# Kernel optimization log

Measured on AMD Instinct MI355X. Metric: run time of the kernel, lower is better.

Reference implementation:

```python
import jax, jax.numpy as jnp
import numpy as np
import math

B, N, E, H = 2, 2048, 1024, 16
D = E // H

def setup_inputs() -> dict:
    key = jax.random.key(0)
    ks = jax.random.split(key, 9)
    s = 1.0 / math.sqrt(E)
    return {
        "x": jax.random.normal(ks[0], (B, N, E), dtype=jnp.float32),
        "Wq": jax.random.uniform(ks[1], (E, E), jnp.float32, -s, s),
        "bq": jax.random.uniform(ks[2], (E,), jnp.float32, -s, s),
        "Wk": jax.random.uniform(ks[3], (E, E), jnp.float32, -s, s),
        "bk": jax.random.uniform(ks[4], (E,), jnp.float32, -s, s),
        "Wv": jax.random.uniform(ks[5], (E, E), jnp.float32, -s, s),
        "bv": jax.random.uniform(ks[6], (E,), jnp.float32, -s, s),
        "Wo": jax.random.uniform(ks[7], (E, E), jnp.float32, -s, s),
        "bo": jax.random.uniform(ks[8], (E,), jnp.float32, -s, s),
    }

def _split_heads(t):
    # [b, n, (h d)] -> [b, h, n, d]
    b, n, _ = t.shape
    return t.reshape(b, n, H, D).transpose(0, 2, 1, 3)

def reference(x, Wq, bq, Wk, bk, Wv, bv, Wo, bo):
    q = _split_heads(x @ Wq.T + bq)
    k = _split_heads(x @ Wk.T + bk)
    v = _split_heads(x @ Wv.T + bv)
    energy = jnp.einsum('bhqd,bhkd->bhqk', q, k)
    # Faithful to source: softmax first, THEN divide by sqrt(n_embedding)
    attention = jax.nn.softmax(energy, axis=-1) / jnp.sqrt(jnp.float32(E))
    out = jnp.einsum('bhqk,bhkd->bhqd', attention, v)
    out = out.transpose(0, 2, 1, 3).reshape(x.shape[0], x.shape[1], E)
    return out @ Wo.T + bo
```

## Files before the change

kernel.cpp:

```cpp
#include <hip/hip_runtime.h>


typedef __bf16 bf16x8 __attribute__((ext_vector_type(8)));
typedef float  f32x4  __attribute__((ext_vector_type(4)));
typedef float  f32x16 __attribute__((ext_vector_type(16)));
using u16 = unsigned short;
using u32 = unsigned int;
typedef u16 u16x8 __attribute__((ext_vector_type(8)));
typedef u16 u16x4 __attribute__((ext_vector_type(4)));
typedef u32 u32x4 __attribute__((ext_vector_type(4)));

constexpr int BATCH = 2, SEQ = 2048, EMB = 1024, NH = 16, HD = 64;
constexpr int MTOT = BATCH * SEQ;
constexpr int KTOT = EMB;
constexpr int NTOT = EMB;
constexpr float LOG2E = 1.44269504088896340736f;

constexpr size_t OFF_XBF = 0;
constexpr size_t OFF_WQ  = 8u * 1024 * 1024;
constexpr size_t OFF_WK  = OFF_WQ + 2u * 1024 * 1024;
constexpr size_t OFF_WV  = OFF_WK + 2u * 1024 * 1024;
constexpr size_t OFF_WO  = OFF_WV + 2u * 1024 * 1024;
constexpr size_t OFF_Q   = OFF_WO + 2u * 1024 * 1024;
constexpr size_t OFF_K   = OFF_Q  + 8u * 1024 * 1024;
constexpr size_t OFF_VT  = OFF_K  + 8u * 1024 * 1024;

__device__ __forceinline__ u16 f2bf(float f) {
  u32 u = __builtin_bit_cast(u32, f);
  u = (u + 0x7fffu + ((u >> 16) & 1u)) >> 16;
  return (u16)u;
}

__device__ __forceinline__ bf16x8 ld_bf16x8(const u16* p) {
  return __builtin_bit_cast(bf16x8, *(const u16x8*)p);
}

__device__ __forceinline__ float fexp2(float x) {
#if __has_builtin(__builtin_amdgcn_exp2f)
  return __builtin_amdgcn_exp2f(x);
#else
  return exp2f(x);
#endif
}

__device__ __forceinline__ float fmax3(float a, float b, float c) {
  float d;
  asm("v_max3_f32 %0, %1, %2, %3" : "=v"(d) : "v"(a), "v"(b), "v"(c));
  return d;
}

__device__ __forceinline__ u32 cvtpk(float lo, float hi_) {
  u32 r;
  asm("v_cvt_pk_bf16_f32 %0, %1, %2" : "=v"(r) : "v"(lo), "v"(hi_));
  return r;
}

__device__ __forceinline__ void stage16(const void* g, void* l) {
#if __has_builtin(__builtin_amdgcn_global_load_lds)
  __builtin_amdgcn_global_load_lds(
      (__attribute__((address_space(1))) void*)const_cast<void*>(g),
      (__attribute__((address_space(3))) void*)l, 16, 0, 0);
#else
  int lane = threadIdx.x & 63;
  uint4 v = *(const uint4*)g;
  *(uint4*)((char*)l + lane * 16) = v;
#endif
}

__global__ __launch_bounds__(256) void cvt_all(
    const float* __restrict__ x, const float* __restrict__ wq,
    const float* __restrict__ wk, const float* __restrict__ wv,
    const float* __restrict__ wo, u16* __restrict__ ox, u16* __restrict__ oq,
    u16* __restrict__ okk, u16* __restrict__ ov, u16* __restrict__ oo) {
  int id = blockIdx.x;
  const float* in;
  u16* out;
  int i;
  if (id < 4096) {
    in = x; out = ox; i = id * 256 + threadIdx.x;
  } else {
    int z = (id - 4096) >> 10, r = (id - 4096) & 1023;
    in = (z == 0) ? wq : (z == 1) ? wk : (z == 2) ? wv : wo;
    out = (z == 0) ? oq : (z == 1) ? okk : (z == 2) ? ov : oo;
    i = r * 256 + threadIdx.x;
  }
  float4 f = ((const float4*)in)[i];
  u32 lo = (u32)f2bf(f.x) | ((u32)f2bf(f.y) << 16);
  u32 hi = (u32)f2bf(f.z) | ((u32)f2bf(f.w) << 16);
  ((uint2*)out)[i] = make_uint2(lo, hi);
}

__device__ __forceinline__ void gemm_bt_core(const u16* __restrict__ A,
                                             const u16* __restrict__ Bm,
                                             const float* __restrict__ bias,
                                             void* __restrict__ out, int mode,
                                             float oscale) {
  __shared__ __align__(16) u16 smem[2][2][128 * 32];
  const int tid = threadIdx.x, w = tid >> 6, ln = tid & 63;
  const int wr = w >> 1, wc = w & 1, qq = ln >> 4, t = ln & 15;
  const int m0 = blockIdx.y * 128, n0 = blockIdx.x * 128;

  f32x4 acc[2][4] = {};

#define GSTAGE(bi, kt)                                                         \
  {                                                                            \
    int ck = w * 64 + ln;                                          \
    int r = ck >> 2, c2 = ck & 3;                                              \
    stage16(&A[(size_t)(m0 + r) * KTOT + (kt) + c2 * 8],                       \
            &smem[bi][0][(size_t)(w * 64) * 8]);                               \
    stage16(&Bm[(size_t)(n0 + r) * KTOT + (kt) + c2 * 8],                      \
            &smem[bi][1][(size_t)(w * 64) * 8]);                               \
  }

  GSTAGE(0, 0)
  __syncthreads();

  int bs = 0;
  for (int kt = 0; kt < KTOT; kt += 32, bs ^= 1) {
    if (kt + 32 < KTOT) GSTAGE(bs ^ 1, kt + 32)
    const u16* sA = smem[bs][0];
    const u16* sB = smem[bs][1];

    bf16x8 av[2], bv[4];
#pragma unroll
    for (int f = 0; f < 2; f++)
      av[f] = ld_bf16x8(&sA[(wr * 32 + f * 16 + t) * 32 + qq * 8]);
#pragma unroll
    for (int f = 0; f < 4; f++)
      bv[f] = ld_bf16x8(&sB[(wc * 64 + f * 16 + t) * 32 + qq * 8]);
#pragma unroll
    for (int i = 0; i < 2; i++)
#pragma unroll
      for (int j = 0; j < 4; j++)
        acc[i][j] = __builtin_amdgcn_mfma_f32_16x16x32_bf16(av[i], bv[j], acc[i][j], 0, 0, 0);
    __syncthreads();
  }
#undef GSTAGE

  if (mode == 1) {
    u16* tb = (u16*)smem;
    const int b = m0 >> 11;
    const int t16 = tid & 15;
    const int tokb = (m0 & 2047) + t16 * 8;
#pragma unroll
    for (int ph = 0; ph < 2; ph++) {
      if (ph == 1) __syncthreads();
      if (wc == ph) {
#pragma unroll
        for (int fc = 0; fc < 4; fc++) {
          int nl = fc * 16 + t;
          float bn = bias[n0 + ph * 64 + nl];
#pragma unroll
          for (int fr = 0; fr < 2; fr++)
#pragma unroll
            for (int i = 0; i < 4; i++) {
              int ml = wr * 32 + fr * 16 + qq * 4 + i;
              tb[nl * 128 + (ml ^ ((nl & 7) << 4))] = f2bf(acc[fr][fc][i] + bn);
            }
        }
      }
      __syncthreads();
#pragma unroll
      for (int p = 0; p < 2; p++) {
        int row = p * 32 + (tid >> 4);
        int n = n0 + ph * 64 + row;
        int hh = n >> 6, d = n & 63;
        u16x8 vd = *(const u16x8*)&tb[row * 128 + ((t16 * 8) ^ ((row & 7) << 4))];
        *(u16x8*)&((u16*)out)[(((size_t)(b * NH + hh)) * HD + d) * SEQ + tokb] = vd;
      }
    }
    return;
  }

#pragma unroll
  for (int fc = 0; fc < 4; fc++) {
    int n = n0 + wc * 64 + fc * 16 + t;
    float bn = bias[n];
#pragma unroll
    for (int fr = 0; fr < 2; fr++) {
#pragma unroll
      for (int i = 0; i < 4; i++) {
        int m = m0 + wr * 32 + fr * 16 + qq * 4 + i;
        float v = (acc[fr][fc][i] + bn) * oscale;
        if (mode == 2) {
          ((float*)out)[(size_t)m * NTOT + n] = v;
        } else {
          int b = m >> 11, tok = m & 2047, h = n >> 6, d = n & 63;
          ((u16*)out)[(((size_t)(b * NH + h)) * SEQ + tok) * HD + d] = f2bf(v);
        }
      }
    }
  }
}

__global__ __launch_bounds__(512) void gemm_qkv(
    const u16* __restrict__ A, const u16* __restrict__ WQ, const u16* __restrict__ WK,
    const u16* __restrict__ WV, const float* __restrict__ bq, const float* __restrict__ bk,
    const float* __restrict__ bv, u16* Qo, u16* Ko, u16* Vo) {
  int z = blockIdx.z;
  const u16* Bm = (z == 0) ? WQ : ((z == 1) ? WK : WV);
  const float* bias = (z == 0) ? bq : ((z == 1) ? bk : bv);
  u16* out = (z == 0) ? Qo : ((z == 1) ? Ko : Vo);
  gemm_bt_core(A, Bm, bias, out, (z == 2) ? 1 : 0, (z == 0) ? LOG2E : 1.0f);
}

__global__ __launch_bounds__(512) void gemm_o(const u16* __restrict__ A,
                                              const u16* __restrict__ WO,
                                              const float* __restrict__ bo,
                                              float* __restrict__ out) {
  gemm_bt_core(A, WO, bo, out, 2, 1.0f);
}

__global__ __launch_bounds__(512, 4) void flash_attn(const u16* __restrict__ Q,
                                                     const u16* __restrict__ Kg,
                                                     const u16* __restrict__ VT,
                                                     u16* __restrict__ O) {
  const int e = blockIdx.x;
  const int xcd = e & 7, slot = e >> 3;
  const int bh = xcd * 4 + (slot & 3);
  const int qt = slot >> 2;

  const int tid = threadIdx.x, w = tid >> 6, ln = tid & 63;
  const int c = ln & 31, hi = ln >> 5;
  const int kb = w >> 2;
  const int q0 = qt * 128 + (w & 3) * 32;

  const u16* Qb = Q + (size_t)bh * SEQ * HD;
  const u16* Kb = Kg + (size_t)bh * SEQ * HD;
  const u16* Vb = VT + (size_t)bh * HD * SEQ;

  __shared__ __align__(16) u16 sK[2][64 * 64];
  __shared__ __align__(16) u16 sV[2][64 * 64];
  __shared__ float2 sml[8][64];

  bf16x8 qf[4];
#pragma unroll
  for (int ks = 0; ks < 4; ks++)
    qf[ks] = ld_bf16x8(&Qb[(size_t)(q0 + c) * HD + ks * 16 + hi * 8]);

  const bf16x8 ones = __builtin_bit_cast(
      bf16x8, (u16x8){0x3f80, 0x3f80, 0x3f80, 0x3f80, 0x3f80, 0x3f80, 0x3f80, 0x3f80});

  f32x16 ot[2];
  ot[0] = 0.f; ot[1] = 0.f;
  f32x16 acc_l = 0.f;
  float m = -1e30f;

#define STAGE(buf, kt)                                                         \
  {                                                                            \
    int ck = w * 64 + ln;                                                      \
    int r = ck >> 3, c2 = ck & 7, c2s = c2 ^ (r & 7);                          \
    stage16(&Kb[(size_t)((kt) + r) * HD + c2s * 8],                            \
            &sK[buf][(size_t)(w * 64) * 8]);                                   \
    stage16(&Vb[(size_t)r * SEQ + (kt) + c2s * 8],                             \
            &sV[buf][(size_t)(w * 64) * 8]);                                   \
  }

  STAGE(0, 0)
  __syncthreads();

  int it = 0;
  for (int kt = 0; kt < SEQ; kt += 64, it ^= 1) {
    if (kt + 64 < SEQ) STAGE(it ^ 1, kt + 64)
    const u16* kbuf = sK[it];
    const u16* vbuf = sV[it];

    f32x16 st = 0.f;
    __builtin_amdgcn_s_setprio(1);
#pragma unroll
    for (int ks = 0; ks < 4; ks++) {
      int row = kb * 32 + c;
      int boff = ((2 * ks + hi) ^ (row & 7)) << 4;
      bf16x8 kf = ld_bf16x8((const u16*)((const char*)(kbuf + row * 64) + boff));
      st = __builtin_amdgcn_mfma_f32_32x32x16_bf16(kf, qf[ks], st, 0, 0, 0);
    }
    __builtin_amdgcn_s_setprio(0);

    float a0 = fmax3(st[0], st[1], st[2]);
    float a1 = fmax3(st[3], st[4], st[5]);
    float a2 = fmax3(st[6], st[7], st[8]);
    float a3 = fmax3(st[9], st[10], st[11]);
    float a4 = fmax3(st[12], st[13], st[14]);
    float a5 = fmaxf(st[15], a0);
    float b0 = fmax3(a1, a2, a3);
    float b1 = fmax3(a4, a5, b0);
    float pmax = fmaxf(b1, __shfl_xor(b1, 32));

    if (!__all(pmax <= m + 8.0f)) {
      float mn = fmaxf(m, pmax);
      float sc = fexp2(m - mn);
      acc_l[0] *= sc;
#pragma unroll
      for (int i = 0; i < 16; i++) { ot[0][i] *= sc; ot[1][i] *= sc; }
      m = mn;
    }

#pragma unroll
    for (int i = 0; i < 16; i++) st[i] = fexp2(st[i] - m);

    bf16x8 pb[2];
#pragma unroll
    for (int ks2 = 0; ks2 < 2; ks2++) {
      const int R0 = 8 * ks2;
      const int R1 = 4 * ((2 * ks2 + 1) & 3);
      u32 X0 = cvtpk(st[R0], st[R0 + 1]);
      u32 X1 = cvtpk(st[R0 + 2], st[R0 + 3]);
      u32 Y0 = cvtpk(st[R1], st[R1 + 1]);
      u32 Y1 = cvtpk(st[R1 + 2], st[R1 + 3]);
      asm("v_permlane32_swap_b32 %0, %1" : "+v"(X0), "+v"(Y0));
      asm("v_permlane32_swap_b32 %0, %1" : "+v"(X1), "+v"(Y1));
      u32x4 wd; wd.x = X0; wd.y = X1; wd.z = Y0; wd.w = Y1;
      pb[ks2] = __builtin_bit_cast(bf16x8, wd);
    }

    __builtin_amdgcn_s_setprio(1);
#pragma unroll
    for (int ks2 = 0; ks2 < 2; ks2++) {
#pragma unroll
      for (int db = 0; db < 2; db++) {
        int row = db * 32 + c;
        int boff = ((kb * 4 + ks2 * 2 + hi) ^ (row & 7)) << 4;
        bf16x8 vf = ld_bf16x8((const u16*)((const char*)(vbuf + row * 64) + boff));
        ot[db] = __builtin_amdgcn_mfma_f32_32x32x16_bf16(vf, pb[ks2], ot[db], 0, 0, 0);
      }
      acc_l = __builtin_amdgcn_mfma_f32_32x32x16_bf16(ones, pb[ks2], acc_l, 0, 0, 0);
    }
    __builtin_amdgcn_s_setprio(0);
    __syncthreads();
  }
#undef STAGE

  float myl = acc_l[0];
  const int pair = w & 3;
  float* xA = (float*)sK;
  float* xB = (float*)sV;
  {
    f32x16 give = (w < 4) ? ot[1] : ot[0];
    *(f32x16*)((w < 4 ? xA : xB) + (size_t)(pair * 64 + ln) * 16) = give;
    sml[w][ln] = make_float2(m, myl);
  }
  __syncthreads();

  float2 po = sml[w ^ 4][ln];
  float M2 = fmaxf(m, po.x);
  float s_me = fexp2(m - M2), s_po = fexp2(po.x - M2);
  float lf = myl * s_me + po.y * s_po;
  float inv = 1.0f / (lf * 32.0f);
  f32x16 oth = *(const f32x16*)((w < 4 ? xB : xA) + (size_t)(pair * 64 + ln) * 16);
  f32x16 own = (w < 4) ? ot[0] : ot[1];
  const int db = (w < 4) ? 0 : 1;

  const int b = bh >> 4, h = bh & 15;
  u16* obase = O + ((size_t)(b * SEQ + q0 + c)) * EMB + h * HD;
#pragma unroll
  for (int g = 0; g < 4; g++) {
    u16x4 pkt;
#pragma unroll
    for (int i = 0; i < 4; i++)
      pkt[i] = f2bf((own[g * 4 + i] * s_me + oth[g * 4 + i] * s_po) * inv);
    *(u16x4*)(obase + db * 32 + g * 8 + hi * 4) = pkt;
  }
}

extern "C" void kernel_launch(void* const* d_in, const int* in_sizes, int n_in,
                              void* d_out, int out_size, void* d_ws, size_t ws_size,
                              hipStream_t stream) {
  const float* x  = (const float*)d_in[0];
  const float* Wq = (const float*)d_in[1];
  const float* bq = (const float*)d_in[2];
  const float* Wk = (const float*)d_in[3];
  const float* bk = (const float*)d_in[4];
  const float* Wv = (const float*)d_in[5];
  const float* bv = (const float*)d_in[6];
  const float* Wo = (const float*)d_in[7];
  const float* bo = (const float*)d_in[8];

  char* ws = (char*)d_ws;
  u16* xbf = (u16*)(ws + OFF_XBF);
  u16* wqb = (u16*)(ws + OFF_WQ);
  u16* wkb = (u16*)(ws + OFF_WK);
  u16* wvb = (u16*)(ws + OFF_WV);
  u16* wob = (u16*)(ws + OFF_WO);
  u16* Qw  = (u16*)(ws + OFF_Q);
  u16* Kw  = (u16*)(ws + OFF_K);
  u16* Vw  = (u16*)(ws + OFF_VT);

  cvt_all<<<dim3(8192), 256, 0, stream>>>(x, Wq, Wk, Wv, Wo, xbf, wqb, wkb, wvb, wob);

  gemm_qkv<<<dim3(NTOT / 128, MTOT / 128, 3), 512, 0, stream>>>(
      xbf, wqb, wkb, wvb, bq, bk, bv, Qw, Kw, Vw);

  flash_attn<<<dim3(512), 512, 0, stream>>>(Qw, Kw, Vw, xbf);

  gemm_o<<<dim3(NTOT / 128, MTOT / 128), 512, 0, stream>>>(xbf, wob, bo, (float*)d_out);
}
```

Measured before the change: 117.6 us.

## Triple-buffer K/V tiles in flash attention with partial vmcnt waits

Changes the K/V LDS staging in the attention kernel from double to triple buffering, so loads run two tiles ahead. The full __syncthreads is replaced with an s_waitcnt vmcnt(2) plus a raw s_barrier, which lets the newest tile's loads stay in flight across iterations, and buffer pointers rotate each step. This aims to hide global-to-LDS load latency. In exchange it uses more LDS, which may cut occupancy at 4 blocks/CU, and it depends on stage16 issuing exactly two counted loads per stage.

```diff
diff --git a/kernel.cpp b/kernel.cpp
--- a/kernel.cpp
+++ b/kernel.cpp
@@ -229,8 +229,8 @@
   const u16* Kb = Kg + (size_t)bh * SEQ * HD;
   const u16* Vb = VT + (size_t)bh * HD * SEQ;
 
-  __shared__ __align__(16) u16 sK[2][64 * 64];
-  __shared__ __align__(16) u16 sV[2][64 * 64];
+  __shared__ __align__(16) u16 sK[3][64 * 64];
+  __shared__ __align__(16) u16 sV[3][64 * 64];
   __shared__ float2 sml[8][64];
 
   bf16x8 qf[4];
@@ -246,24 +246,24 @@
   f32x16 acc_l = 0.f;
   float m = -1e30f;
 
-#define STAGE(buf, kt)                                                         \
+#define STAGE(pK, pV, kt)                                                      \
   {                                                                            \
     int ck = w * 64 + ln;                                                      \
     int r = ck >> 3, c2 = ck & 7, c2s = c2 ^ (r & 7);                          \
-    stage16(&Kb[(size_t)((kt) + r) * HD + c2s * 8],                            \
-            &sK[buf][(size_t)(w * 64) * 8]);                                   \
-    stage16(&Vb[(size_t)r * SEQ + (kt) + c2s * 8],                             \
-            &sV[buf][(size_t)(w * 64) * 8]);                                   \
-  }
-
-  STAGE(0, 0)
-  __syncthreads();
-
-  int it = 0;
-  for (int kt = 0; kt < SEQ; kt += 64, it ^= 1) {
-    if (kt + 64 < SEQ) STAGE(it ^ 1, kt + 64)
-    const u16* kbuf = sK[it];
-    const u16* vbuf = sV[it];
+    stage16(&Kb[(size_t)((kt) + r) * HD + c2s * 8], (pK) + (size_t)(w * 64) * 8); \
+    stage16(&Vb[(size_t)r * SEQ + (kt) + c2s * 8], (pV) + (size_t)(w * 64) * 8);  \
+  }
+
+  u16 *k0 = sK[0], *k1 = sK[1], *k2 = sK[2];
+  u16 *v0 = sV[0], *v1 = sV[1], *v2 = sV[2];
+
+  STAGE(k0, v0, 0)
+  STAGE(k1, v1, 64)
+  asm volatile("s_waitcnt vmcnt(2)" ::: "memory");
+  __builtin_amdgcn_s_barrier();
+
+  for (int t = 0; t < 32; ++t) {
+    if (t + 2 < 32) STAGE(k2, v2, (t + 2) * 64)
 
     f32x16 st = 0.f;
     __builtin_amdgcn_s_setprio(1);
@@ -271,7 +271,7 @@
     for (int ks = 0; ks < 4; ks++) {
       int row = kb * 32 + c;
       int boff = ((2 * ks + hi) ^ (row & 7)) << 4;
-      bf16x8 kf = ld_bf16x8((const u16*)((const char*)(kbuf + row * 64) + boff));
+      bf16x8 kf = ld_bf16x8((const u16*)((const char*)(k0 + row * 64) + boff));
       st = __builtin_amdgcn_mfma_f32_32x32x16_bf16(kf, qf[ks], st, 0, 0, 0);
     }
     __builtin_amdgcn_s_setprio(0);
@@ -320,13 +320,21 @@
       for (int db = 0; db < 2; db++) {
         int row = db * 32 + c;
         int boff = ((kb * 4 + ks2 * 2 + hi) ^ (row & 7)) << 4;
-        bf16x8 vf = ld_bf16x8((const u16*)((const char*)(vbuf + row * 64) + boff));
+        bf16x8 vf = ld_bf16x8((const u16*)((const char*)(v0 + row * 64) + boff));
         ot[db] = __builtin_amdgcn_mfma_f32_32x32x16_bf16(vf, pb[ks2], ot[db], 0, 0, 0);
       }
       acc_l = __builtin_amdgcn_mfma_f32_32x32x16_bf16(ones, pb[ks2], acc_l, 0, 0, 0);
     }
     __builtin_amdgcn_s_setprio(0);
-    __syncthreads();
+
+    if (t + 2 < 32)
+      asm volatile("s_waitcnt vmcnt(2)" ::: "memory");
+    else if (t == 30)
+      asm volatile("s_waitcnt vmcnt(0)" ::: "memory");
+    __builtin_amdgcn_s_barrier();
+
+    u16* tk = k0; k0 = k1; k1 = k2; k2 = tk;
+    u16* tv = v0; v0 = v1; v1 = v2; v2 = tv;
   }
 #undef STAGE
 
```

After: 116.6 us. No clear change (-0.8%).
